# Kernel tuning notes

Measured on AMD Instinct MI355X. Metric: run time of the kernel, lower is better.

The kernel has to match this reference:

```python
import jax, jax.numpy as jnp
import numpy as np

N, M, B = 1024, 8192, 8192  # W: [N, M], x: [B, N]
BLOCK = 32


def activation_quant(x):
    # per-tensor symmetric int8 fake-quant with STE
    scale = 127.0 / jnp.clip(jnp.max(jnp.abs(x)), 1e-8, None)
    x_q = jnp.clip(jnp.round(x * scale), -128.0, 127.0) / scale
    return x + jax.lax.stop_gradient(x_q - x)


def weight_quant_q2_k(w, block_size=BLOCK):
    # blockwise 2-bit quant with top-2 outliers kept at 4-bit, STE
    shape = w.shape
    wf = w.reshape(-1)
    n = wf.shape[0]
    pad = (-n) % block_size
    wf = jnp.pad(wf, (0, pad))
    blocks = wf.reshape(-1, block_size)
    scales = jnp.clip(jnp.max(jnp.abs(blocks), axis=1, keepdims=True), 1e-8, None)
    nb = blocks / scales
    k = min(2, block_size)
    _, top_idx = jax.lax.top_k(jnp.abs(nb), k)
    rows = jnp.arange(nb.shape[0])[:, None]
    top_mask = jnp.zeros(nb.shape, dtype=bool).at[rows, top_idx].set(True)
    q4 = jnp.round(nb * 7.0) / 7.0
    abs_nb = jnp.abs(nb)
    q2 = jnp.sign(nb) * jnp.where(abs_nb > 0.66, 1.0, 1.0 / 3.0)
    q = jnp.where(top_mask, q4, q2) * scales
    w_q = q.reshape(-1)[:n].reshape(shape)
    return w + jax.lax.stop_gradient(w_q - w)


def setup_inputs() -> dict:
    key = jax.random.key(0)
    k1, k2, k3 = jax.random.split(key, 3)
    x = jax.random.normal(k1, (B, N), dtype=jnp.float32)
    W = jax.random.normal(k2, (N, M), dtype=jnp.float32) / np.float32(np.sqrt(M))
    b = jax.random.normal(k3, (N,), dtype=jnp.float32)
    idx = jnp.arange(M // 2, dtype=jnp.int32)            # expanded (quantized) columns
    idx_comp = jnp.arange(M // 2, M, dtype=jnp.int32)    # continuous columns
    return {"x": x, "W": W, "b": b, "idx": idx, "idx_comp": idx_comp}


def reference(x, W, b, idx, idx_comp):
    W_exp_q = weight_quant_q2_k(jnp.take(W, idx, axis=1))   # [N, M/2]
    W_cont = jnp.take(W, idx_comp, axis=1)                  # [N, M/2]
    hidden_exp = activation_quant(x) @ W_exp_q              # [B, M/2]
    hidden_cont = x @ W_cont                                # [B, M/2]
    hidden = (jnp.zeros((x.shape[0], M), dtype=x.dtype)
              .at[:, idx].set(hidden_exp)
              .at[:, idx_comp].set(hidden_cont))            # scatter back to [B, M]
    h_exp = activation_quant(hidden[:, idx])
    out = jax.nn.relu(h_exp @ W_exp_q.T + hidden[:, idx_comp] @ W_cont.T + b)
    return out
```

## Files before the change

### kernel.cpp

```cpp
#include <hip/hip_runtime.h>
#include <hip/hip_bf16.h>
#include <cstdint>


using bf16x8 = __attribute__((ext_vector_type(8))) __bf16;
using f32x4  = __attribute__((ext_vector_type(4))) float;

typedef const __attribute__((address_space(1))) void g_void;
typedef __attribute__((address_space(3))) void l_void;

__device__ __forceinline__ void gload16(const void* g, void* l) {
  __builtin_amdgcn_global_load_lds((g_void*)g, (l_void*)l, 16, 0, 0);
}

__device__ __forceinline__ ushort f2bf(float f) {
  union { float f; unsigned u; } c; c.f = f;
  unsigned r = c.u + 0x7FFFu + ((c.u >> 16) & 1u);
  return (ushort)(r >> 16);
}
__device__ __forceinline__ float bf2f(ushort u) {
  union { unsigned u; float f; } c; c.u = ((unsigned)u) << 16;
  return c.f;
}

__global__ void prep_wa_kernel(const float* __restrict__ W,
                               const float4* __restrict__ x,
                               ushort* __restrict__ Wq,
                               ushort* __restrict__ WqT,
                               ushort* __restrict__ Wcb,
                               unsigned* __restrict__ amax_bits) {
  const int bidx = blockIdx.x;
  const int tid = threadIdx.x;

  if (bidx < 1024) {
    __shared__ __align__(16) ushort tile[64][72];
    const int rt = bidx >> 6;
    const int ct = bidx & 63;
    const int r0 = rt * 64, c0 = ct * 64;
    const int e = tid & 31;
    const int hw = tid >> 5;
    #pragma unroll
    for (int it = 0; it < 16; ++it) {
      const int g = it * 8 + hw;
      const int row = g >> 1;
      const int cg = (g & 1) * 32;
      const float w = W[(size_t)(r0 + row) * 8192 + c0 + cg + e];
      float aw = fabsf(w);
      float m = aw;
      #pragma unroll
      for (int d = 1; d <= 16; d <<= 1) m = fmaxf(m, __shfl_xor(m, d));
      int idx = (aw == m) ? e : 32;
      #pragma unroll
      for (int d = 1; d <= 16; d <<= 1) idx = min(idx, __shfl_xor(idx, d));
      const int i1 = idx;
      float a2 = (e == i1) ? -1.f : aw;
      float m2 = a2;
      #pragma unroll
      for (int d = 1; d <= 16; d <<= 1) m2 = fmaxf(m2, __shfl_xor(m2, d));
      int idx2 = (a2 == m2) ? e : 32;
      #pragma unroll
      for (int d = 1; d <= 16; d <<= 1) idx2 = min(idx2, __shfl_xor(idx2, d));
      const int i2 = idx2;

      const float scale = fmaxf(m, 1e-8f);
      const float nb = w / scale;
      float q;
      if (e == i1 || e == i2) {
        q = rintf(nb * 7.f) / 7.f;
      } else {
        float s = (nb > 0.f) ? 1.f : ((nb < 0.f) ? -1.f : 0.f);
        q = s * ((fabsf(nb) > 0.66f) ? 1.f : (1.f / 3.f));
      }
      const ushort qb = f2bf(q * scale);
      Wq[(size_t)(r0 + row) * 4096 + c0 + cg + e] = qb;
      tile[cg + e][row] = qb;
    }
    __syncthreads();
    const int c = tid >> 2;
    const int q4 = (tid & 3) * 16;
    uint4 v0 = *(const uint4*)&tile[c][q4];
    uint4 v1 = *(const uint4*)&tile[c][q4 + 8];
    *(uint4*)(WqT + (size_t)(c0 + c) * 1024 + r0 + q4) = v0;
    *(uint4*)(WqT + (size_t)(c0 + c) * 1024 + r0 + q4 + 8) = v1;
  } else if (bidx < 5120) {
    const int u = (bidx - 1024) * 256 + tid;
    const int row = u >> 10;
    const int c4 = u & 1023;
    float4 v = *(const float4*)(W + (size_t)row * 8192 + 4096 + c4 * 4);
    ushort4 o;
    o.x = f2bf(v.x); o.y = f2bf(v.y); o.z = f2bf(v.z); o.w = f2bf(v.w);
    *(ushort4*)(Wcb + (size_t)row * 4096 + c4 * 4) = o;
  } else {
    float m = 0.f;
    const int base = (bidx - 5120) * 256 + tid;
    const int stride = 2048 * 256;
    for (int i = base; i < 8192 * 1024 / 4; i += stride) {
      float4 v = x[i];
      m = fmaxf(m, fmaxf(fmaxf(fabsf(v.x), fabsf(v.y)),
                         fmaxf(fabsf(v.z), fabsf(v.w))));
    }
    #pragma unroll
    for (int off = 32; off > 0; off >>= 1) m = fmaxf(m, __shfl_down(m, off));
    __shared__ float wm[4];
    int lane = tid & 63, wave = tid >> 6;
    if (lane == 0) wm[wave] = m;
    __syncthreads();
    if (tid == 0) {
      float r = fmaxf(fmaxf(wm[0], wm[1]), fmaxf(wm[2], wm[3]));
      atomicMax(amax_bits, __float_as_uint(r));
    }
  }
}

__global__ void prep_x_kernel(const float4* __restrict__ x,
                              const unsigned* __restrict__ amax_bits,
                              uint4* __restrict__ xq, uint4* __restrict__ xbf) {
  const float amax = fmaxf(__uint_as_float(*amax_bits), 1e-8f);
  const float scale = 127.f / amax;
  const int base = blockIdx.x * 256 + threadIdx.x;
  const int stride = 2048 * 256;
  const int n8 = 8192 * 1024 / 8;
  for (int i = base; i < n8; i += stride) {
    float4 a = x[i * 2], b = x[i * 2 + 1];
    float v[8] = {a.x, a.y, a.z, a.w, b.x, b.y, b.z, b.w};
    unsigned qw[4], bw[4];
    #pragma unroll
    for (int j = 0; j < 4; ++j) {
      float q0 = fminf(fmaxf(rintf(v[2 * j] * scale), -128.f), 127.f) / scale;
      float q1 = fminf(fmaxf(rintf(v[2 * j + 1] * scale), -128.f), 127.f) / scale;
      qw[j] = (unsigned)f2bf(q0) | ((unsigned)f2bf(q1) << 16);
      bw[j] = (unsigned)f2bf(v[2 * j]) | ((unsigned)f2bf(v[2 * j + 1]) << 16);
    }
    xq[i] = make_uint4(qw[0], qw[1], qw[2], qw[3]);
    xbf[i] = make_uint4(bw[0], bw[1], bw[2], bw[3]);
  }
}

__global__ __launch_bounds__(256, 2) void gemm1_kernel(
    const ushort* __restrict__ Wcb,
    ushort* __restrict__ G,
    const ushort* __restrict__ Aq, const ushort* __restrict__ BT,
    ushort* __restrict__ Hexp, unsigned* __restrict__ amax_bits) {
  __shared__ __align__(16) ushort As[2][128 * 32];
  __shared__ __align__(16) ushort Bs[2][128 * 32];
  __shared__ float wredmax[4];

  const int bidx = blockIdx.x;
  const int tid = threadIdx.x;
  const int lane = tid & 63, wave = tid >> 6;
  const int l15 = lane & 15, quad = lane >> 4;
  const int wm = (wave >> 1) << 6, wn = (wave & 1) << 6;

  ushort* Asl0 = As[0] + tid * 8; ushort* Asl1 = As[1] + tid * 8;
  ushort* Bsl0 = Bs[0] + tid * 8; ushort* Bsl1 = Bs[1] + tid * 8;

  f32x4 acc[4][4];
  #pragma unroll
  for (int i = 0; i < 4; ++i)
    #pragma unroll
    for (int j = 0; j < 4; ++j) acc[i][j] = (f32x4){0.f, 0.f, 0.f, 0.f};

  if (bidx < 64) {
    const int gy = bidx >> 3, gx = bidx & 7;
    const int i0 = gy * 128, j0 = gx * 128;
    const ushort* Ag = Wcb + (size_t)(i0 + (tid >> 2)) * 4096 + (tid & 3) * 8;
    const ushort* Bg = Wcb + (size_t)(j0 + (tid >> 2)) * 4096 + (tid & 3) * 8;
    for (int k0 = 0; k0 < 4096; k0 += 64) {
      __syncthreads();
      gload16(Ag + k0, Asl0);
      gload16(Ag + (size_t)64 * 4096 + k0, Asl0 + 64 * 32);
      gload16(Bg + k0, Bsl0);
      gload16(Bg + (size_t)64 * 4096 + k0, Bsl0 + 64 * 32);
      gload16(Ag + k0 + 32, Asl1);
      gload16(Ag + (size_t)64 * 4096 + k0 + 32, Asl1 + 64 * 32);
      gload16(Bg + k0 + 32, Bsl1);
      gload16(Bg + (size_t)64 * 4096 + k0 + 32, Bsl1 + 64 * 32);
      __syncthreads();
      #pragma unroll
      for (int p = 0; p < 2; ++p) {
        bf16x8 af[4], bfr[4];
        #pragma unroll
        for (int i = 0; i < 4; ++i)
          af[i] = *(const bf16x8*)&As[p][(wm + i * 16 + l15) * 32 + quad * 8];
        #pragma unroll
        for (int j = 0; j < 4; ++j)
          bfr[j] = *(const bf16x8*)&Bs[p][(wn + j * 16 + l15) * 32 + quad * 8];
        #pragma unroll
        for (int i = 0; i < 4; ++i)
          #pragma unroll
          for (int j = 0; j < 4; ++j)
            acc[i][j] = __builtin_amdgcn_mfma_f32_16x16x32_bf16(af[i], bfr[j], acc[i][j], 0, 0, 0);
      }
    }
    const int row0 = i0 + wm + quad * 4;
    const int col0 = j0 + wn + l15;
    #pragma unroll
    for (int i = 0; i < 4; ++i)
      #pragma unroll
      for (int j = 0; j < 4; ++j)
        #pragma unroll
        for (int r = 0; r < 4; ++r)
          G[(size_t)(row0 + i * 16 + r) * 1024 + (col0 + j * 16)] = f2bf(acc[i][j][r]);
    return;
  }

  const int l = bidx - 64;
  const int xcd = l & 7;
  const int s = l >> 3;
  const int t = (xcd << 2) | (s >> 6);
  const int u = s & 63;
  const int bx = ((t & 3) << 3) | (u & 7);
  const int by = ((t >> 2) << 3) | (u >> 3);

  const ushort* Ag = Aq + (size_t)(by * 128 + (tid >> 2)) * 1024 + (tid & 3) * 8;
  const ushort* Bg = BT + (size_t)(bx * 128 + (tid >> 2)) * 1024 + (tid & 3) * 8;

  for (int k0 = 0; k0 < 1024; k0 += 64) {
    __syncthreads();
    gload16(Ag + k0, Asl0);
    gload16(Ag + 64 * 1024 + k0, Asl0 + 64 * 32);
    gload16(Bg + k0, Bsl0);
    gload16(Bg + 64 * 1024 + k0, Bsl0 + 64 * 32);
    gload16(Ag + k0 + 32, Asl1);
    gload16(Ag + 64 * 1024 + k0 + 32, Asl1 + 64 * 32);
    gload16(Bg + k0 + 32, Bsl1);
    gload16(Bg + 64 * 1024 + k0 + 32, Bsl1 + 64 * 32);
    __syncthreads();

    #pragma unroll
    for (int p = 0; p < 2; ++p) {
      bf16x8 af[4], bfr[4];
      #pragma unroll
      for (int i = 0; i < 4; ++i)
        af[i] = *(const bf16x8*)&As[p][(wm + i * 16 + l15) * 32 + quad * 8];
      #pragma unroll
      for (int j = 0; j < 4; ++j)
        bfr[j] = *(const bf16x8*)&Bs[p][(wn + j * 16 + l15) * 32 + quad * 8];
      #pragma unroll
      for (int i = 0; i < 4; ++i)
        #pragma unroll
        for (int j = 0; j < 4; ++j)
          acc[i][j] = __builtin_amdgcn_mfma_f32_16x16x32_bf16(af[i], bfr[j], acc[i][j], 0, 0, 0);
    }
  }

  const int row0 = by * 128 + wm + quad * 4;
  const int col0 = bx * 128 + wn + l15;
  float lmax = 0.f;
  #pragma unroll
  for (int i = 0; i < 4; ++i)
    #pragma unroll
    for (int j = 0; j < 4; ++j)
      #pragma unroll
      for (int r = 0; r < 4; ++r) {
        float v = acc[i][j][r];
        lmax = fmaxf(lmax, fabsf(v));
        Hexp[(size_t)(row0 + i * 16 + r) * 4096 + (col0 + j * 16)] = f2bf(v);
      }

  #pragma unroll
  for (int off = 32; off > 0; off >>= 1)
    lmax = fmaxf(lmax, __shfl_down(lmax, off));
  if (lane == 0) wredmax[wave] = lmax;
  __syncthreads();
  if (tid == 0) {
    float m = fmaxf(fmaxf(wredmax[0], wredmax[1]), fmaxf(wredmax[2], wredmax[3]));
    atomicMax(amax_bits, __float_as_uint(m));
  }
}

__global__ void quant_h_kernel(ushort* __restrict__ H,
                               const unsigned* __restrict__ amax_bits) {
  const float amax = fmaxf(__uint_as_float(*amax_bits), 1e-8f);
  const float scale = 127.f / amax;
  const int n8 = 8192 * 4096 / 8;
  for (int i = blockIdx.x * blockDim.x + threadIdx.x; i < n8;
       i += gridDim.x * blockDim.x) {
    uint4* p = (uint4*)H + i;
    uint4 a = *p;
    unsigned w[4] = {a.x, a.y, a.z, a.w};
    #pragma unroll
    for (int j = 0; j < 4; ++j) {
      float lo = bf2f((ushort)(w[j] & 0xFFFF));
      float hi = bf2f((ushort)(w[j] >> 16));
      lo = fminf(fmaxf(rintf(lo * scale), -128.f), 127.f) / scale;
      hi = fminf(fmaxf(rintf(hi * scale), -128.f), 127.f) / scale;
      w[j] = (unsigned)f2bf(lo) | ((unsigned)f2bf(hi) << 16);
    }
    *p = make_uint4(w[0], w[1], w[2], w[3]);
  }
}

__global__ __launch_bounds__(256, 2) void gemm2_kernel(
    const ushort* __restrict__ Hq, const ushort* __restrict__ Wq,
    const ushort* __restrict__ Xb, const ushort* __restrict__ G,
    const float* __restrict__ bias, float* __restrict__ out) {
  __shared__ __align__(16) ushort As[2][128 * 32];
  __shared__ __align__(16) ushort Bs[2][128 * 32];

  const int l = blockIdx.x;
  const int xcd = l & 7;
  const int s = l >> 3;
  const int by = (xcd << 3) | (s >> 3);
  const int bx = s & 7;

  const int tid = threadIdx.x;
  const int lane = tid & 63, wave = tid >> 6;
  const int wm = (wave >> 1) << 6, wn = (wave & 1) << 6;
  const int l15 = lane & 15, quad = lane >> 4;

  ushort* Asl0 = As[0] + tid * 8; ushort* Asl1 = As[1] + tid * 8;
  ushort* Bsl0 = Bs[0] + tid * 8; ushort* Bsl1 = Bs[1] + tid * 8;

  f32x4 acc[4][4];
  #pragma unroll
  for (int i = 0; i < 4; ++i)
    #pragma unroll
    for (int j = 0; j < 4; ++j) acc[i][j] = (f32x4){0.f, 0.f, 0.f, 0.f};

  {
    const ushort* Ag = Hq + (size_t)(by * 128 + (tid >> 2)) * 4096 + (tid & 3) * 8;
    const ushort* Bg = Wq + (size_t)(bx * 128 + (tid >> 2)) * 4096 + (tid & 3) * 8;
    for (int k0 = 0; k0 < 4096; k0 += 64) {
      __syncthreads();
      gload16(Ag + k0, Asl0);
      gload16(Ag + (size_t)64 * 4096 + k0, Asl0 + 64 * 32);
      gload16(Bg + k0, Bsl0);
      gload16(Bg + (size_t)64 * 4096 + k0, Bsl0 + 64 * 32);
      gload16(Ag + k0 + 32, Asl1);
      gload16(Ag + (size_t)64 * 4096 + k0 + 32, Asl1 + 64 * 32);
      gload16(Bg + k0 + 32, Bsl1);
      gload16(Bg + (size_t)64 * 4096 + k0 + 32, Bsl1 + 64 * 32);
      __syncthreads();
      #pragma unroll
      for (int p = 0; p < 2; ++p) {
        bf16x8 af[4], bfr[4];
        #pragma unroll
        for (int i = 0; i < 4; ++i)
          af[i] = *(const bf16x8*)&As[p][(wm + i * 16 + l15) * 32 + quad * 8];
        #pragma unroll
        for (int j = 0; j < 4; ++j)
          bfr[j] = *(const bf16x8*)&Bs[p][(wn + j * 16 + l15) * 32 + quad * 8];
        #pragma unroll
        for (int i = 0; i < 4; ++i)
          #pragma unroll
          for (int j = 0; j < 4; ++j)
            acc[i][j] = __builtin_amdgcn_mfma_f32_16x16x32_bf16(af[i], bfr[j], acc[i][j], 0, 0, 0);
      }
    }
  }
  {
    const ushort* Ag = Xb + (size_t)(by * 128 + (tid >> 2)) * 1024 + (tid & 3) * 8;
    const ushort* Bg = G + (size_t)(bx * 128 + (tid >> 2)) * 1024 + (tid & 3) * 8;
    for (int k0 = 0; k0 < 1024; k0 += 64) {
      __syncthreads();
      gload16(Ag + k0, Asl0);
      gload16(Ag + 64 * 1024 + k0, Asl0 + 64 * 32);
      gload16(Bg + k0, Bsl0);
      gload16(Bg + 64 * 1024 + k0, Bsl0 + 64 * 32);
      gload16(Ag + k0 + 32, Asl1);
      gload16(Ag + 64 * 1024 + k0 + 32, Asl1 + 64 * 32);
      gload16(Bg + k0 + 32, Bsl1);
      gload16(Bg + 64 * 1024 + k0 + 32, Bsl1 + 64 * 32);
      __syncthreads();
      #pragma unroll
      for (int p = 0; p < 2; ++p) {
        bf16x8 af[4], bfr[4];
        #pragma unroll
        for (int i = 0; i < 4; ++i)
          af[i] = *(const bf16x8*)&As[p][(wm + i * 16 + l15) * 32 + quad * 8];
        #pragma unroll
        for (int j = 0; j < 4; ++j)
          bfr[j] = *(const bf16x8*)&Bs[p][(wn + j * 16 + l15) * 32 + quad * 8];
        #pragma unroll
        for (int i = 0; i < 4; ++i)
          #pragma unroll
          for (int j = 0; j < 4; ++j)
            acc[i][j] = __builtin_amdgcn_mfma_f32_16x16x32_bf16(af[i], bfr[j], acc[i][j], 0, 0, 0);
      }
    }
  }

  const int row0 = by * 128 + wm + quad * 4;
  const int col0 = bx * 128 + wn + l15;
  #pragma unroll
  for (int i = 0; i < 4; ++i)
    #pragma unroll
    for (int j = 0; j < 4; ++j) {
      float bv = bias[col0 + j * 16];
      #pragma unroll
      for (int r = 0; r < 4; ++r) {
        float v = acc[i][j][r] + bv;
        v = fmaxf(v, 0.f);
        out[(size_t)(row0 + i * 16 + r) * 1024 + (col0 + j * 16)] = v;
      }
    }
}

extern "C" void kernel_launch(void* const* d_in, const int* in_sizes, int n_in,
                              void* d_out, int out_size, void* d_ws, size_t ws_size,
                              hipStream_t stream) {
  (void)in_sizes; (void)n_in; (void)out_size; (void)ws_size;
  const float* x = (const float*)d_in[0];
  const float* W = (const float*)d_in[1];
  const float* b = (const float*)d_in[2];

  char* ws = (char*)d_ws;
  unsigned* scal = (unsigned*)ws;
  ushort* xq   = (ushort*)(ws + 256);
  ushort* xbf  = xq   + (size_t)8192 * 1024;
  ushort* Wq   = xbf  + (size_t)8192 * 1024;
  ushort* WqT  = Wq   + (size_t)1024 * 4096;
  ushort* Wcb  = WqT  + (size_t)4096 * 1024;
  ushort* G    = Wcb  + (size_t)1024 * 4096;
  ushort* Hexp = G    + (size_t)1024 * 1024;

  hipMemsetAsync(scal, 0, 256, stream);
  prep_wa_kernel<<<7168, 256, 0, stream>>>(W, (const float4*)x, Wq, WqT, Wcb, scal);
  prep_x_kernel<<<2048, 256, 0, stream>>>((const float4*)x, scal,
                                          (uint4*)xq, (uint4*)xbf);
  gemm1_kernel<<<2112, 256, 0, stream>>>(Wcb, G, xq, WqT, Hexp, scal + 1);
  quant_h_kernel<<<4096, 256, 0, stream>>>(Hexp, scal + 1);
  gemm2_kernel<<<512, 256, 0, stream>>>(Hexp, Wq, xbf, G, b, (float*)d_out);
}
```

Measured before the change: 342.3 us.

## Rewrite GEMMs with 8-wave 256-tile, multi-stage LDS pipeline and swizzled layout

Both GEMM kernels move to 512-thread blocks with larger output tiles (256x256 for gemm1, 256x128 for gemm2). They use a shared pipelined loop that keeps three k-stages of global-to-LDS loads in flight, using explicit vmcnt waits, s_barrier and setprio instead of the full __syncthreads pairs. LDS reads and writes are XOR-swizzled to avoid bank conflicts. The goal is to hide memory latency and raise MFMA utilisation. In exchange it uses 128 KB of LDS per block and more accumulators, which can limit occupancy and adds pipeline-correctness risk.

Result: slower. 498.0 us (+45.5%).

```diff
diff --git a/kernel.cpp b/kernel.cpp
--- a/kernel.cpp
+++ b/kernel.cpp
@@ -21,6 +21,17 @@
 __device__ __forceinline__ float bf2f(ushort u) {
   union { unsigned u; float f; } c; c.u = ((unsigned)u) << 16;
   return c.f;
+}
+
+template <int N>
+__device__ __forceinline__ void wait_vmcnt() {
+  static_assert(N == 0 || N == 2 || N == 3 || N == 4 || N == 6 || N == 8, "");
+  if constexpr (N == 0) asm volatile("s_waitcnt vmcnt(0)" ::: "memory");
+  else if constexpr (N == 2) asm volatile("s_waitcnt vmcnt(2)" ::: "memory");
+  else if constexpr (N == 3) asm volatile("s_waitcnt vmcnt(3)" ::: "memory");
+  else if constexpr (N == 4) asm volatile("s_waitcnt vmcnt(4)" ::: "memory");
+  else if constexpr (N == 6) asm volatile("s_waitcnt vmcnt(6)" ::: "memory");
+  else if constexpr (N == 8) asm volatile("s_waitcnt vmcnt(8)" ::: "memory");
 }
 
 __global__ void prep_wa_kernel(const float* __restrict__ W,
@@ -136,135 +147,144 @@
   }
 }
 
-__global__ __launch_bounds__(256, 2) void gemm1_kernel(
-    const ushort* __restrict__ Wcb,
-    ushort* __restrict__ G,
+template <int FI, int FJ, int OPG, class STAGE>
+__device__ __forceinline__ void pipe2(ushort (&As)[32768], ushort (&Bs)[32768],
+                                      const int NG, STAGE&& stage,
+                                      f32x4 (&acc)[FI][FJ],
+                                      const int aoff0, const int boff0) {
+  constexpr int ASTR = FI * 2048;
+  constexpr int BSTR = FJ * 1024;
+  stage(0); stage(1); stage(2);
+  wait_vmcnt<2 * OPG>();
+  __builtin_amdgcn_s_barrier();
+  auto phase = [&](int p, int buf, int kk) {
+    __builtin_amdgcn_sched_barrier(0);
+    const ushort* Ab = &As[buf * (2 * ASTR) + kk * ASTR];
+    const ushort* Bb = &Bs[buf * (2 * BSTR) + kk * BSTR];
+    bf16x8 af[FI]; bf16x8 bfr[FJ];
+    #pragma unroll
+    for (int i = 0; i < FI; ++i)
+      af[i] = *(const bf16x8*)(Ab + aoff0 + i * 512);
+    #pragma unroll
+    for (int j = 0; j < FJ; ++j)
+      bfr[j] = *(const bf16x8*)(Bb + boff0 + j * 512);
+    if (p + 3 < NG) stage(p + 3);
+    __builtin_amdgcn_s_barrier();
+    __builtin_amdgcn_s_setprio(1);
+    #pragma unroll
+    for (int i = 0; i < FI; ++i)
+      #pragma unroll
+      for (int j = 0; j < FJ; ++j)
+        acc[i][j] = __builtin_amdgcn_mfma_f32_16x16x32_bf16(af[i], bfr[j],
+                                                            acc[i][j], 0, 0, 0);
+    __builtin_amdgcn_s_setprio(0);
+    if (p < NG - 3) wait_vmcnt<2 * OPG>();
+    else if (p == NG - 3) wait_vmcnt<OPG>();
+    else if (p == NG - 2) wait_vmcnt<0>();
+    __builtin_amdgcn_s_barrier();
+  };
+  for (int p0 = 0; p0 < NG; p0 += 4) {
+    phase(p0 + 0, 0, 0);
+    phase(p0 + 1, 0, 1);
+    phase(p0 + 2, 1, 0);
+    phase(p0 + 3, 1, 1);
+  }
+}
+
+__global__ __launch_bounds__(512, 2) void gemm1_kernel(
+    const ushort* __restrict__ Wcb, ushort* __restrict__ G,
     const ushort* __restrict__ Aq, const ushort* __restrict__ BT,
     ushort* __restrict__ Hexp, unsigned* __restrict__ amax_bits) {
-  __shared__ __align__(16) ushort As[2][128 * 32];
-  __shared__ __align__(16) ushort Bs[2][128 * 32];
-  __shared__ float wredmax[4];
-
-  const int bidx = blockIdx.x;
+  __shared__ __align__(16) ushort As[32768];
+  __shared__ __align__(16) ushort Bs[32768];
+  __shared__ float wred[8];
   const int tid = threadIdx.x;
   const int lane = tid & 63, wave = tid >> 6;
-  const int l15 = lane & 15, quad = lane >> 4;
-  const int wm = (wave >> 1) << 6, wn = (wave & 1) << 6;
-
-  ushort* Asl0 = As[0] + tid * 8; ushort* Asl1 = As[1] + tid * 8;
-  ushort* Bsl0 = Bs[0] + tid * 8; ushort* Bsl1 = Bs[1] + tid * 8;
-
-  f32x4 acc[4][4];
-  #pragma unroll
-  for (int i = 0; i < 4; ++i)
-    #pragma unroll
-    for (int j = 0; j < 4; ++j) acc[i][j] = (f32x4){0.f, 0.f, 0.f, 0.f};
-
-  if (bidx < 64) {
-    const int gy = bidx >> 3, gx = bidx & 7;
-    const int i0 = gy * 128, j0 = gx * 128;
-    const ushort* Ag = Wcb + (size_t)(i0 + (tid >> 2)) * 4096 + (tid & 3) * 8;
-    const ushort* Bg = Wcb + (size_t)(j0 + (tid >> 2)) * 4096 + (tid & 3) * 8;
-    for (int k0 = 0; k0 < 4096; k0 += 64) {
-      __syncthreads();
-      gload16(Ag + k0, Asl0);
-      gload16(Ag + (size_t)64 * 4096 + k0, Asl0 + 64 * 32);
-      gload16(Bg + k0, Bsl0);
-      gload16(Bg + (size_t)64 * 4096 + k0, Bsl0 + 64 * 32);
-      gload16(Ag + k0 + 32, Asl1);
-      gload16(Ag + (size_t)64 * 4096 + k0 + 32, Asl1 + 64 * 32);
-      gload16(Bg + k0 + 32, Bsl1);
-      gload16(Bg + (size_t)64 * 4096 + k0 + 32, Bsl1 + 64 * 32);
-      __syncthreads();
-      #pragma unroll
-      for (int p = 0; p < 2; ++p) {
-        bf16x8 af[4], bfr[4];
-        #pragma unroll
-        for (int i = 0; i < 4; ++i)
-          af[i] = *(const bf16x8*)&As[p][(wm + i * 16 + l15) * 32 + quad * 8];
-        #pragma unroll
-        for (int j = 0; j < 4; ++j)
-          bfr[j] = *(const bf16x8*)&Bs[p][(wn + j * 16 + l15) * 32 + quad * 8];
-        #pragma unroll
-        for (int i = 0; i < 4; ++i)
-          #pragma unroll
-          for (int j = 0; j < 4; ++j)
-            acc[i][j] = __builtin_amdgcn_mfma_f32_16x16x32_bf16(af[i], bfr[j], acc[i][j], 0, 0, 0);
-      }
-    }
-    const int row0 = i0 + wm + quad * 4;
-    const int col0 = j0 + wn + l15;
-    #pragma unroll
-    for (int i = 0; i < 4; ++i)
+  const int wm = wave >> 1, wn = wave & 1;
+  const int l15 = lane & 15, quad = (lane >> 4) & 3;
+  const int sel = (quad ^ ((l15 >> 1) & 3)) * 8;
+  const int scs = ((tid & 3) ^ ((tid >> 3) & 3)) * 8;
+  const int rsrc = tid >> 2;
+  const int l = blockIdx.x;
+
+  if (l < 64) {
+    const int by = l >> 3, bx = l & 7;
+    const ushort* aB = Wcb + (size_t)(by * 128 + rsrc) * 4096 + scs;
+    const ushort* bB = Wcb + (size_t)(bx * 128 + rsrc) * 4096 + scs;
+    f32x4 acc[2][4];
+    #pragma unroll
+    for (int i = 0; i < 2; ++i)
+      #pragma unroll
+      for (int j = 0; j < 4; ++j) acc[i][j] = (f32x4){0.f, 0.f, 0.f, 0.f};
+    const int aoff0 = (wm * 32 + l15) * 32 + sel;
+    const int boff0 = (wn * 64 + l15) * 32 + sel;
+    auto stage = [&](int g) {
+      const int t = g >> 1, kk = g & 1, buf = t & 1;
+      const int koff = t * 64 + kk * 32;
+      gload16(aB + koff, &As[buf * 8192 + kk * 4096 + tid * 8]);
+      gload16(bB + koff, &Bs[buf * 8192 + kk * 4096 + tid * 8]);
+    };
+    pipe2<2, 4, 2>(As, Bs, 128, stage, acc, aoff0, boff0);
+    const int row0 = by * 128 + wm * 32 + quad * 4;
+    const int col0 = bx * 128 + wn * 64 + l15;
+    #pragma unroll
+    for (int i = 0; i < 2; ++i)
       #pragma unroll
       for (int j = 0; j < 4; ++j)
         #pragma unroll
         for (int r = 0; r < 4; ++r)
-          G[(size_t)(row0 + i * 16 + r) * 1024 + (col0 + j * 16)] = f2bf(acc[i][j][r]);
+          G[(size_t)(row0 + i * 16 + r) * 1024 + (col0 + j * 16)] =
+              f2bf(acc[i][j][r]);
     return;
   }
 
-  const int l = bidx - 64;
-  const int xcd = l & 7;
-  const int s = l >> 3;
-  const int t = (xcd << 2) | (s >> 6);
-  const int u = s & 63;
-  const int bx = ((t & 3) << 3) | (u & 7);
-  const int by = ((t >> 2) << 3) | (u >> 3);
-
-  const ushort* Ag = Aq + (size_t)(by * 128 + (tid >> 2)) * 1024 + (tid & 3) * 8;
-  const ushort* Bg = BT + (size_t)(bx * 128 + (tid >> 2)) * 1024 + (tid & 3) * 8;
-
-  for (int k0 = 0; k0 < 1024; k0 += 64) {
-    __syncthreads();
-    gload16(Ag + k0, Asl0);
-    gload16(Ag + 64 * 1024 + k0, Asl0 + 64 * 32);
-    gload16(Bg + k0, Bsl0);
-    gload16(Bg + 64 * 1024 + k0, Bsl0 + 64 * 32);
-    gload16(Ag + k0 + 32, Asl1);
-    gload16(Ag + 64 * 1024 + k0 + 32, Asl1 + 64 * 32);
-    gload16(Bg + k0 + 32, Bsl1);
-    gload16(Bg + 64 * 1024 + k0 + 32, Bsl1 + 64 * 32);
-    __syncthreads();
-
-    #pragma unroll
-    for (int p = 0; p < 2; ++p) {
-      bf16x8 af[4], bfr[4];
-      #pragma unroll
-      for (int i = 0; i < 4; ++i)
-        af[i] = *(const bf16x8*)&As[p][(wm + i * 16 + l15) * 32 + quad * 8];
-      #pragma unroll
-      for (int j = 0; j < 4; ++j)
-        bfr[j] = *(const bf16x8*)&Bs[p][(wn + j * 16 + l15) * 32 + quad * 8];
-      #pragma unroll
-      for (int i = 0; i < 4; ++i)
-        #pragma unroll
-        for (int j = 0; j < 4; ++j)
-          acc[i][j] = __builtin_amdgcn_mfma_f32_16x16x32_bf16(af[i], bfr[j], acc[i][j], 0, 0, 0);
-    }
-  }
-
-  const int row0 = by * 128 + wm + quad * 4;
-  const int col0 = bx * 128 + wn + l15;
+  const int lg = l - 64;
+  const int wgid = (lg & 7) * 64 + (lg >> 3);
+  const int by = wgid >> 4, bx = wgid & 15;
+
+  const ushort* aB = Aq + (size_t)(by * 256 + rsrc) * 1024 + scs;
+  const ushort* bB = BT + (size_t)(bx * 256 + rsrc) * 1024 + scs;
+  f32x4 acc[4][8];
+  #pragma unroll
+  for (int i = 0; i < 4; ++i)
+    #pragma unroll
+    for (int j = 0; j < 8; ++j) acc[i][j] = (f32x4){0.f, 0.f, 0.f, 0.f};
+  const int aoff0 = (wm * 64 + l15) * 32 + sel;
+  const int boff0 = (wn * 128 + l15) * 32 + sel;
+  auto stage = [&](int g) {
+    const int t = g >> 1, kk = g & 1, buf = t & 1;
+    const int koff = t * 64 + kk * 32;
+    ushort* ad = &As[buf * 16384 + kk * 8192 + tid * 8];
+    gload16(aB + koff, ad);
+    gload16(aB + 131072 + koff, ad + 4096);
+    ushort* bd = &Bs[buf * 16384 + kk * 8192 + tid * 8];
+    gload16(bB + koff, bd);
+    gload16(bB + 131072 + koff, bd + 4096);
+  };
+  pipe2<4, 8, 4>(As, Bs, 32, stage, acc, aoff0, boff0);
+
+  const int row0 = by * 256 + wm * 64 + quad * 4;
+  const int col0 = bx * 256 + wn * 128 + l15;
   float lmax = 0.f;
   #pragma unroll
   for (int i = 0; i < 4; ++i)
     #pragma unroll
-    for (int j = 0; j < 4; ++j)
+    for (int j = 0; j < 8; ++j)
       #pragma unroll
       for (int r = 0; r < 4; ++r) {
         float v = acc[i][j][r];
         lmax = fmaxf(lmax, fabsf(v));
         Hexp[(size_t)(row0 + i * 16 + r) * 4096 + (col0 + j * 16)] = f2bf(v);
       }
-
   #pragma unroll
   for (int off = 32; off > 0; off >>= 1)
     lmax = fmaxf(lmax, __shfl_down(lmax, off));
-  if (lane == 0) wredmax[wave] = lmax;
+  if (lane == 0) wred[wave] = lmax;
   __syncthreads();
   if (tid == 0) {
-    float m = fmaxf(fmaxf(wredmax[0], wredmax[1]), fmaxf(wredmax[2], wredmax[3]));
+    float m = wred[0];
+    #pragma unroll
+    for (int i = 1; i < 8; ++i) m = fmaxf(m, wred[i]);
     atomicMax(amax_bits, __float_as_uint(m));
   }
 }
@@ -291,98 +311,57 @@
   }
 }
 
-__global__ __launch_bounds__(256, 2) void gemm2_kernel(
+__global__ __launch_bounds__(512, 2) void gemm2_kernel(
     const ushort* __restrict__ Hq, const ushort* __restrict__ Wq,
-    const ushort* __restrict__ Xb, const ushort* __restrict__ G,
+    const ushort* __restrict__ Xb, const ushort* __restrict__ Gm,
     const float* __restrict__ bias, float* __restrict__ out) {
-  __shared__ __align__(16) ushort As[2][128 * 32];
-  __shared__ __align__(16) ushort Bs[2][128 * 32];
-
-  const int l = blockIdx.x;
-  const int xcd = l & 7;
-  const int s = l >> 3;
-  const int by = (xcd << 3) | (s >> 3);
-  const int bx = s & 7;
-
+  __shared__ __align__(16) ushort As[32768];
+  __shared__ __align__(16) ushort Bs[32768];
   const int tid = threadIdx.x;
   const int lane = tid & 63, wave = tid >> 6;
-  const int wm = (wave >> 1) << 6, wn = (wave & 1) << 6;
-  const int l15 = lane & 15, quad = lane >> 4;
-
-  ushort* Asl0 = As[0] + tid * 8; ushort* Asl1 = As[1] + tid * 8;
-  ushort* Bsl0 = Bs[0] + tid * 8; ushort* Bsl1 = Bs[1] + tid * 8;
+  const int wm = wave >> 1, wn = wave & 1;
+  const int l15 = lane & 15, quad = (lane >> 4) & 3;
+  const int sel = (quad ^ ((l15 >> 1) & 3)) * 8;
+  const int scs = ((tid & 3) ^ ((tid >> 3) & 3)) * 8;
+  const int rsrc = tid >> 2;
+
+  const int l = blockIdx.x;
+  const int wgid = (l & 7) * 32 + (l >> 3);
+  const int by = wgid >> 3, bx = wgid & 7;
+
+  const ushort* a1 = Hq + (size_t)(by * 256 + rsrc) * 4096 + scs;
+  const ushort* a2 = Xb + (size_t)(by * 256 + rsrc) * 1024 + scs;
+  const ushort* b1 = Wq + (size_t)(bx * 128 + rsrc) * 4096 + scs;
+  const ushort* b2 = Gm + (size_t)(bx * 128 + rsrc) * 1024 + scs;
 
   f32x4 acc[4][4];
   #pragma unroll
   for (int i = 0; i < 4; ++i)
     #pragma unroll
     for (int j = 0; j < 4; ++j) acc[i][j] = (f32x4){0.f, 0.f, 0.f, 0.f};
-
-  {
-    const ushort* Ag = Hq + (size_t)(by * 128 + (tid >> 2)) * 4096 + (tid & 3) * 8;
-    const ushort* Bg = Wq + (size_t)(bx * 128 + (tid >> 2)) * 4096 + (tid & 3) * 8;
-    for (int k0 = 0; k0 < 4096; k0 += 64) {
-      __syncthreads();
-      gload16(Ag + k0, Asl0);
-      gload16(Ag + (size_t)64 * 4096 + k0, Asl0 + 64 * 32);
-      gload16(Bg + k0, Bsl0);
-      gload16(Bg + (size_t)64 * 4096 + k0, Bsl0 + 64 * 32);
-      gload16(Ag + k0 + 32, Asl1);
-      gload16(Ag + (size_t)64 * 4096 + k0 + 32, Asl1 + 64 * 32);
-      gload16(Bg + k0 + 32, Bsl1);
-      gload16(Bg + (size_t)64 * 4096 + k0 + 32, Bsl1 + 64 * 32);
-      __syncthreads();
-      #pragma unroll
-      for (int p = 0; p < 2; ++p) {
-        bf16x8 af[4], bfr[4];
-        #pragma unroll
-        for (int i = 0; i < 4; ++i)
-          af[i] = *(const bf16x8*)&As[p][(wm + i * 16 + l15) * 32 + quad * 8];
-        #pragma unroll
-        for (int j = 0; j < 4; ++j)
-          bfr[j] = *(const bf16x8*)&Bs[p][(wn + j * 16 + l15) * 32 + quad * 8];
-        #pragma unroll
-        for (int i = 0; i < 4; ++i)
-          #pragma unroll
-          for (int j = 0; j < 4; ++j)
-            acc[i][j] = __builtin_amdgcn_mfma_f32_16x16x32_bf16(af[i], bfr[j], acc[i][j], 0, 0, 0);
-      }
-    }
-  }
-  {
-    const ushort* Ag = Xb + (size_t)(by * 128 + (tid >> 2)) * 1024 + (tid & 3) * 8;
-    const ushort* Bg = G + (size_t)(bx * 128 + (tid >> 2)) * 1024 + (tid & 3) * 8;
-    for (int k0 = 0; k0 < 1024; k0 += 64) {
-      __syncthreads();
-      gload16(Ag + k0, Asl0);
-      gload16(Ag + 64 * 1024 + k0, Asl0 + 64 * 32);
-      gload16(Bg + k0, Bsl0);
-      gload16(Bg + 64 * 1024 + k0, Bsl0 + 64 * 32);
-      gload16(Ag + k0 + 32, Asl1);
-      gload16(Ag + 64 * 1024 + k0 + 32, Asl1 + 64 * 32);
-      gload16(Bg + k0 + 32, Bsl1);
-      gload16(Bg + 64 * 1024 + k0 + 32, Bsl1 + 64 * 32);
-      __syncthreads();
-      #pragma unroll
-      for (int p = 0; p < 2; ++p) {
-        bf16x8 af[4], bfr[4];
-        #pragma unroll
-        for (int i = 0; i < 4; ++i)
-          af[i] = *(const bf16x8*)&As[p][(wm + i * 16 + l15) * 32 + quad * 8];
-        #pragma unroll
-        for (int j = 0; j < 4; ++j)
-          bfr[j] = *(const bf16x8*)&Bs[p][(wn + j * 16 + l15) * 32 + quad * 8];
-        #pragma unroll
-        for (int i = 0; i < 4; ++i)
-          #pragma unroll
-          for (int j = 0; j < 4; ++j)
-            acc[i][j] = __builtin_amdgcn_mfma_f32_16x16x32_bf16(af[i], bfr[j], acc[i][j], 0, 0, 0);
-      }
-    }
-  }
-
-  const int row0 = by * 128 + wm + quad * 4;
-  const int col0 = bx * 128 + wn + l15;
+  const int aoff0 = (wm * 64 + l15) * 32 + sel;
+  const int boff0 = (wn * 64 + l15) * 32 + sel;
+
+  auto stage = [&](int g) {
+    const int t = g >> 1, kk = g & 1, buf = t & 1;
+    ushort* ad = &As[buf * 16384 + kk * 8192 + tid * 8];
+    ushort* bd = &Bs[buf * 8192 + kk * 4096 + tid * 8];
+    if (t < 64) {
+      const int koff = t * 64 + kk * 32;
+      gload16(a1 + koff, ad);
+      gload16(a1 + (size_t)524288 + koff, ad + 4096);
+      gload16(b1 + koff, bd);
+    } else {
+      const int koff = (t - 64) * 64 + kk * 32;
+      gload16(a2 + koff, ad);
+      gload16(a2 + 131072 + koff, ad + 4096);
+      gload16(b2 + koff, bd);
+    }
+  };
+  pipe2<4, 4, 3>(As, Bs, 160, stage, acc, aoff0, boff0);
+
+  const int row0 = by * 256 + wm * 64 + quad * 4;
+  const int col0 = bx * 128 + wn * 64 + l15;
   #pragma unroll
   for (int i = 0; i < 4; ++i)
     #pragma unroll
@@ -419,7 +398,7 @@
   prep_wa_kernel<<<7168, 256, 0, stream>>>(W, (const float4*)x, Wq, WqT, Wcb, scal);
   prep_x_kernel<<<2048, 256, 0, stream>>>((const float4*)x, scal,
                                           (uint4*)xq, (uint4*)xbf);
-  gemm1_kernel<<<2112, 256, 0, stream>>>(Wcb, G, xq, WqT, Hexp, scal + 1);
+  gemm1_kernel<<<576, 512, 0, stream>>>(Wcb, G, xq, WqT, Hexp, scal + 1);
   quant_h_kernel<<<4096, 256, 0, stream>>>(Hexp, scal + 1);
-  gemm2_kernel<<<512, 256, 0, stream>>>(Hexp, Wq, xbf, G, b, (float*)d_out);
-}
+  gemm2_kernel<<<256, 512, 0, stream>>>(Hexp, Wq, xbf, G, b, (float*)d_out);
+}
```
